# Performance work log

Measured on AMD Instinct MI355X. Metric: run time of the kernel, lower is better.

## Reference

```python
import jax, jax.numpy as jnp
import numpy as np

N = 50000        # nodes
E = 640000       # edges
D = 128          # emb_dim
L = 3            # num_layer
EDGE_DIM = 8
BN_EPS = 1e-5


def setup_inputs() -> dict:
    key = jax.random.key(0)
    ks = jax.random.split(key, 6)
    return dict(
        x=jax.random.normal(ks[0], (N, D), jnp.float32),
        edge_index=jax.random.randint(ks[1], (2, E), 0, N),
        edge_attr=jax.random.normal(ks[2], (E, EDGE_DIM), jnp.float32),
        eps=jnp.zeros((L,), jnp.float32),
        We=jax.random.normal(ks[3], (L, EDGE_DIM, D), jnp.float32) * 0.1,
        be=jnp.zeros((L, D), jnp.float32),
        W1=jax.random.normal(ks[4], (L, D, 2 * D), jnp.float32) * (1.0 / np.sqrt(D)),
        b1=jnp.zeros((L, 2 * D), jnp.float32),
        g1=jnp.ones((L, 2 * D), jnp.float32),
        bt1=jnp.zeros((L, 2 * D), jnp.float32),
        W2=jax.random.normal(ks[5], (L, 2 * D, D), jnp.float32) * (1.0 / np.sqrt(2 * D)),
        b2=jnp.zeros((L, D), jnp.float32),
        gbn=jnp.ones((L, D), jnp.float32),
        bbn=jnp.zeros((L, D), jnp.float32),
    )


def _bn(h, g, b):
    # BatchNorm1d, training-mode statistics over the node/batch axis
    mu = h.mean(axis=0)
    var = h.var(axis=0)
    return (h - mu) * jax.lax.rsqrt(var + BN_EPS) * g + b


def reference(x, edge_index, edge_attr, eps, We, be, W1, b1, g1, bt1, W2, b2, gbn, bbn):
    src, dst = edge_index[0], edge_index[1]
    h = x
    for l in range(L):
        # GINConv: edge-encoded messages, relu, scatter-add aggregation
        ee = edge_attr @ We[l] + be[l]                      # [E, D]
        msg = jax.nn.relu(h[src] + ee)                      # [E, D]
        agg = jax.ops.segment_sum(msg, dst, num_segments=N)  # [N, D]
        z = (1.0 + eps[l]) * h + agg
        # GIN MLP: Linear -> BN -> ReLU -> Linear
        z = jax.nn.relu(_bn(z @ W1[l] + b1[l], g1[l], bt1[l]))
        z = z @ W2[l] + b2[l]
        # outer per-layer BatchNorm; ReLU on all but the last layer (dropout = eval identity)
        z = _bn(z, gbn[l], bbn[l])
        if l < L - 1:
            z = jax.nn.relu(z)
        h = z  # residual=False, so no skip add
    return h  # JK == 'last'
```

## Files before the change

### kernel.cpp

```cpp
#include <hip/hip_runtime.h>

#define N_NODES 50000
#define N_EDGES 640000
#define D 128
#define D2 256
#define BN_EPS 1e-5f

typedef unsigned short ushort_t;
typedef unsigned int uint_t;

using bf16x8 = __attribute__((ext_vector_type(8))) short;
using f32x4  = __attribute__((ext_vector_type(4))) float;

__device__ inline ushort_t f2bf(float f) {
    uint_t u = __builtin_bit_cast(uint_t, f);
    u = (u + 0x7fffu + ((u >> 16) & 1u)) >> 16;
    return (ushort_t)u;
}
__device__ inline float bf2f(uint_t bits_lo16) {
    return __builtin_bit_cast(float, bits_lo16 << 16);
}

__global__ __launch_bounds__(256) void hist_kernel(
    const int* __restrict__ dst, int* __restrict__ hist)
{
    const int e = blockIdx.x * 256 + threadIdx.x;
    if (e < N_EDGES) atomicAdd(&hist[dst[e]], 1);
}

__global__ __launch_bounds__(256) void scan1_kernel(
    const int* __restrict__ hist, int* __restrict__ scanA,
    int* __restrict__ bsum)
{
    __shared__ int sm[256];
    const int t = threadIdx.x;
    const int idx = blockIdx.x * 256 + t;
    int val = (idx < N_NODES) ? hist[idx] : 0;
    sm[t] = val;
    __syncthreads();
#pragma unroll
    for (int off = 1; off < 256; off <<= 1) {
        const int add = (t >= off) ? sm[t - off] : 0;
        __syncthreads();
        val += add;
        sm[t] = val;
        __syncthreads();
    }
    scanA[idx] = val;
    if (t == 255) bsum[blockIdx.x] = val;
}

__global__ __launch_bounds__(256) void scan2_kernel(
    const int* __restrict__ bsum, int* __restrict__ bscan, int nb)
{
    __shared__ int sm[256];
    const int t = threadIdx.x;
    int val = (t < nb) ? bsum[t] : 0;
    sm[t] = val;
    __syncthreads();
#pragma unroll
    for (int off = 1; off < 256; off <<= 1) {
        const int add = (t >= off) ? sm[t - off] : 0;
        __syncthreads();
        val += add;
        sm[t] = val;
        __syncthreads();
    }
    bscan[t] = val;
}

__global__ __launch_bounds__(256) void scan3_kernel(
    const int* __restrict__ hist, const int* __restrict__ scanA,
    const int* __restrict__ bscan, int* __restrict__ excl)
{
    const int idx = blockIdx.x * 256 + threadIdx.x;
    if (idx < N_NODES) {
        const int carry = blockIdx.x ? bscan[blockIdx.x - 1] : 0;
        const int incl = scanA[idx] + carry;
        excl[idx] = incl - hist[idx];
        if (idx == N_NODES - 1) excl[N_NODES] = incl;
    }
}

__global__ __launch_bounds__(256) void scatter_kernel(
    const int* __restrict__ src, const int* __restrict__ dst,
    int* __restrict__ cursor, int* __restrict__ srcp_s,
    int* __restrict__ eperm)
{
    const int e = blockIdx.x * 256 + threadIdx.x;
    if (e < N_EDGES) {
        const int t = dst[e];
        const int p = atomicAdd(&cursor[t], 1);
        srcp_s[p] = src[e];
        eperm[p] = e;
    }
}

__global__ __launch_bounds__(256) void wtrans_kernel(
    const float* __restrict__ in, ushort_t* __restrict__ out, int K, int Nt)
{
    __shared__ float tile[32][33];
    const int l = blockIdx.z;
    in  += (size_t)l * K * Nt;
    out += (size_t)l * K * Nt;
    const int n0 = blockIdx.x * 32, k0 = blockIdx.y * 32;
    const int tx = threadIdx.x & 31, ty = threadIdx.x >> 5;
#pragma unroll
    for (int i = 0; i < 32; i += 8)
        tile[ty + i][tx] = in[(size_t)(k0 + ty + i) * Nt + n0 + tx];
    __syncthreads();
#pragma unroll
    for (int i = 0; i < 32; i += 8)
        out[(size_t)(n0 + ty + i) * K + k0 + tx] = f2bf(tile[tx][ty + i]);
}

__global__ __launch_bounds__(256) void agg_z_kernel(
    const float* __restrict__ h, const int* __restrict__ excl,
    const int* __restrict__ srcp_s, const int* __restrict__ eperm,
    const float* __restrict__ ea, const float* __restrict__ We_l,
    const float* __restrict__ be_l, const float* __restrict__ eps_l,
    ushort_t* __restrict__ z)
{
    const int lane = threadIdx.x & 63;
    const int wave = threadIdx.x >> 6;
    const int node = blockIdx.x * 4 + wave;
    const int grp  = lane >> 4;
    const int gl   = lane & 15;
    const int d0   = gl * 8;

    float wv[8][8];
#pragma unroll
    for (int k = 0; k < 8; ++k) {
        *(float4*)&wv[k][0] = *(const float4*)&We_l[k * D + d0];
        *(float4*)&wv[k][4] = *(const float4*)&We_l[k * D + d0 + 4];
    }
    float bev[8];
    *(float4*)&bev[0] = *(const float4*)&be_l[d0];
    *(float4*)&bev[4] = *(const float4*)&be_l[d0 + 4];

    const int p0 = excl[node];
    const int p1 = excl[node + 1];
    float acc[8] = {0.f, 0.f, 0.f, 0.f, 0.f, 0.f, 0.f, 0.f};

    for (int p = p0 + grp; p < p1; p += 4) {
        const int e = eperm[p];
        const int s = srcp_s[p];
        float eav[8];
        *(float4*)&eav[0] = *(const float4*)&ea[(size_t)e * 8];
        *(float4*)&eav[4] = *(const float4*)&ea[(size_t)e * 8 + 4];
        float hv[8];
        *(float4*)&hv[0] = *(const float4*)&h[(size_t)s * D + d0];
        *(float4*)&hv[4] = *(const float4*)&h[(size_t)s * D + d0 + 4];
        float m[8];
#pragma unroll
        for (int j = 0; j < 8; ++j) m[j] = bev[j];
#pragma unroll
        for (int k = 0; k < 8; ++k)
#pragma unroll
            for (int j = 0; j < 8; ++j)
                m[j] = fmaf(eav[k], wv[k][j], m[j]);
#pragma unroll
        for (int j = 0; j < 8; ++j)
            acc[j] += fmaxf(hv[j] + m[j], 0.f);
    }

#pragma unroll
    for (int j = 0; j < 8; ++j) {
        acc[j] += __shfl_xor(acc[j], 16);
        acc[j] += __shfl_xor(acc[j], 32);
    }

    if (grp == 0) {
        const float epsv = 1.0f + eps_l[0];
        float hn[8];
        *(float4*)&hn[0] = *(const float4*)&h[(size_t)node * D + d0];
        *(float4*)&hn[4] = *(const float4*)&h[(size_t)node * D + d0 + 4];
        uint4 o;
        uint_t w0 = (uint_t)f2bf(fmaf(epsv, hn[0], acc[0]));
        uint_t w1 = (uint_t)f2bf(fmaf(epsv, hn[1], acc[1]));
        uint_t w2 = (uint_t)f2bf(fmaf(epsv, hn[2], acc[2]));
        uint_t w3 = (uint_t)f2bf(fmaf(epsv, hn[3], acc[3]));
        uint_t w4 = (uint_t)f2bf(fmaf(epsv, hn[4], acc[4]));
        uint_t w5 = (uint_t)f2bf(fmaf(epsv, hn[5], acc[5]));
        uint_t w6 = (uint_t)f2bf(fmaf(epsv, hn[6], acc[6]));
        uint_t w7 = (uint_t)f2bf(fmaf(epsv, hn[7], acc[7]));
        o.x = w0 | (w1 << 16);
        o.y = w2 | (w3 << 16);
        o.z = w4 | (w5 << 16);
        o.w = w6 | (w7 << 16);
        *(uint4*)&z[(size_t)node * D + d0] = o;
    }
}

template<int KTILES>
__global__ __launch_bounds__(256) void gemm_bf16_kernel(
    const ushort_t* __restrict__ A, const ushort_t* __restrict__ Bt,
    const float* __restrict__ bias, ushort_t* __restrict__ out,
    float* __restrict__ gsum, float* __restrict__ gsq)
{
    __shared__ ushort_t As[128][136];
    __shared__ ushort_t Bs[128][136];
    __shared__ float ls_sum[128], ls_sq[128];
    const int tid = threadIdx.x;
    const int M0 = blockIdx.x * 128;
    const int N0 = blockIdx.y * 128;
    const int Ntot = gridDim.y * 128;
    const int K = KTILES * 128;
    if (tid < 128) { ls_sum[tid] = 0.f; ls_sq[tid] = 0.f; }
    const int lane = tid & 63, w = tid >> 6;
    const int wm = w >> 1, wn = w & 1;
    const int lr = lane & 15;
    const int lk = (lane >> 4) * 8;
    f32x4 acc[4][4] = {};

    for (int kt = 0; kt < KTILES; ++kt) {
        if (kt) __syncthreads();
#pragma unroll
        for (int p = 0; p < 8; ++p) {
            const int idx = p * 256 + tid;
            const int row = idx >> 4, ch = (idx & 15) * 8;
            uint4 v = make_uint4(0, 0, 0, 0);
            const int gr = M0 + row;
            if (gr < N_NODES)
                v = *(const uint4*)&A[(size_t)gr * K + kt * 128 + ch];
            *(uint4*)&As[row][ch] = v;
        }
#pragma unroll
        for (int p = 0; p < 8; ++p) {
            const int idx = p * 256 + tid;
            const int row = idx >> 4, ch = (idx & 15) * 8;
            *(uint4*)&Bs[row][ch] =
                *(const uint4*)&Bt[(size_t)(N0 + row) * K + kt * 128 + ch];
        }
        __syncthreads();
#pragma unroll
        for (int ks = 0; ks < 4; ++ks) {
            const int kof = ks * 32 + lk;
            bf16x8 af[4], bfr[4];
#pragma unroll
            for (int mi = 0; mi < 4; ++mi)
                af[mi] = *(const bf16x8*)&As[wm * 64 + mi * 16 + lr][kof];
#pragma unroll
            for (int ni = 0; ni < 4; ++ni)
                bfr[ni] = *(const bf16x8*)&Bs[wn * 64 + ni * 16 + lr][kof];
#pragma unroll
            for (int mi = 0; mi < 4; ++mi)
#pragma unroll
                for (int ni = 0; ni < 4; ++ni)
                    acc[mi][ni] = __builtin_amdgcn_mfma_f32_16x16x32_bf16(
                        af[mi], bfr[ni], acc[mi][ni], 0, 0, 0);
        }
    }
    __syncthreads();

#pragma unroll
    for (int ni = 0; ni < 4; ++ni) {
        const int cl = wn * 64 + ni * 16 + lr;
        const float bv = bias[N0 + cl];
        float ps = 0.f, pq = 0.f;
#pragma unroll
        for (int mi = 0; mi < 4; ++mi) {
            const int rbase = M0 + wm * 64 + mi * 16 + (lane >> 4) * 4;
#pragma unroll
            for (int r = 0; r < 4; ++r) {
                const int row = rbase + r;
                if (row < N_NODES) {
                    const float v = acc[mi][ni][r] + bv;
                    out[(size_t)row * Ntot + N0 + cl] = f2bf(v);
                    ps += v;
                    pq += v * v;
                }
            }
        }
        atomicAdd(&ls_sum[cl], ps);
        atomicAdd(&ls_sq[cl], pq);
    }
    __syncthreads();
    if (tid < 128) {
        unsafeAtomicAdd(&gsum[N0 + tid], ls_sum[tid]);
        unsafeAtomicAdd(&gsq[N0 + tid], ls_sq[tid]);
    }
}

__global__ void bnparam_kernel(const float* __restrict__ gsum,
                               const float* __restrict__ gsq,
                               const float* __restrict__ g,
                               const float* __restrict__ bt,
                               float* __restrict__ scale,
                               float* __restrict__ shift, int C)
{
    const int c = threadIdx.x;
    if (c < C) {
        const float inv_n = 1.0f / (float)N_NODES;
        const float mu = gsum[c] * inv_n;
        const float var = gsq[c] * inv_n - mu * mu;
        const float s = g[c] * rsqrtf(var + BN_EPS);
        scale[c] = s;
        shift[c] = bt[c] - mu * s;
    }
}

__global__ __launch_bounds__(256) void bnapply1_kernel(
    const ushort_t* __restrict__ t, const float* __restrict__ sc,
    const float* __restrict__ sh, ushort_t* __restrict__ u)
{
    const size_t idx = (size_t)blockIdx.x * 256 + threadIdx.x;
    const int c = (int)(idx & 31) * 8;
    const uint4 v = ((const uint4*)t)[idx];
    const float4 s0 = *(const float4*)&sc[c];
    const float4 s1 = *(const float4*)&sc[c + 4];
    const float4 h0 = *(const float4*)&sh[c];
    const float4 h1 = *(const float4*)&sh[c + 4];
    float f[8];
    f[0] = bf2f(v.x & 0xffffu); f[1] = bf2f(v.x >> 16);
    f[2] = bf2f(v.y & 0xffffu); f[3] = bf2f(v.y >> 16);
    f[4] = bf2f(v.z & 0xffffu); f[5] = bf2f(v.z >> 16);
    f[6] = bf2f(v.w & 0xffffu); f[7] = bf2f(v.w >> 16);
    f[0] = fmaxf(fmaf(f[0], s0.x, h0.x), 0.f);
    f[1] = fmaxf(fmaf(f[1], s0.y, h0.y), 0.f);
    f[2] = fmaxf(fmaf(f[2], s0.z, h0.z), 0.f);
    f[3] = fmaxf(fmaf(f[3], s0.w, h0.w), 0.f);
    f[4] = fmaxf(fmaf(f[4], s1.x, h1.x), 0.f);
    f[5] = fmaxf(fmaf(f[5], s1.y, h1.y), 0.f);
    f[6] = fmaxf(fmaf(f[6], s1.z, h1.z), 0.f);
    f[7] = fmaxf(fmaf(f[7], s1.w, h1.w), 0.f);
    uint4 o;
    o.x = (uint_t)f2bf(f[0]) | ((uint_t)f2bf(f[1]) << 16);
    o.y = (uint_t)f2bf(f[2]) | ((uint_t)f2bf(f[3]) << 16);
    o.z = (uint_t)f2bf(f[4]) | ((uint_t)f2bf(f[5]) << 16);
    o.w = (uint_t)f2bf(f[6]) | ((uint_t)f2bf(f[7]) << 16);
    ((uint4*)u)[idx] = o;
}

__global__ __launch_bounds__(256) void bnapply2_kernel(
    const ushort_t* __restrict__ t, const float* __restrict__ sc,
    const float* __restrict__ sh, float* __restrict__ outp, const int relu)
{
    const size_t idx = (size_t)blockIdx.x * 256 + threadIdx.x;
    const int c = (int)(idx & 15) * 8;
    const uint4 v = ((const uint4*)t)[idx];
    const float4 s0 = *(const float4*)&sc[c];
    const float4 s1 = *(const float4*)&sc[c + 4];
    const float4 h0 = *(const float4*)&sh[c];
    const float4 h1 = *(const float4*)&sh[c + 4];
    float4 r0, r1;
    r0.x = fmaf(bf2f(v.x & 0xffffu), s0.x, h0.x);
    r0.y = fmaf(bf2f(v.x >> 16),     s0.y, h0.y);
    r0.z = fmaf(bf2f(v.y & 0xffffu), s0.z, h0.z);
    r0.w = fmaf(bf2f(v.y >> 16),     s0.w, h0.w);
    r1.x = fmaf(bf2f(v.z & 0xffffu), s1.x, h1.x);
    r1.y = fmaf(bf2f(v.z >> 16),     s1.y, h1.y);
    r1.z = fmaf(bf2f(v.w & 0xffffu), s1.z, h1.z);
    r1.w = fmaf(bf2f(v.w >> 16),     s1.w, h1.w);
    if (relu) {
        r0.x = fmaxf(r0.x, 0.f); r0.y = fmaxf(r0.y, 0.f);
        r0.z = fmaxf(r0.z, 0.f); r0.w = fmaxf(r0.w, 0.f);
        r1.x = fmaxf(r1.x, 0.f); r1.y = fmaxf(r1.y, 0.f);
        r1.z = fmaxf(r1.z, 0.f); r1.w = fmaxf(r1.w, 0.f);
    }
    *(float4*)&outp[idx * 8]     = r0;
    *(float4*)&outp[idx * 8 + 4] = r1;
}

extern "C" void kernel_launch(void* const* d_in, const int* in_sizes, int n_in,
                              void* d_out, int out_size, void* d_ws, size_t ws_size,
                              hipStream_t stream)
{
    const float* x         = (const float*)d_in[0];
    const int*   edge_index= (const int*)d_in[1];
    const float* edge_attr = (const float*)d_in[2];
    const float* eps       = (const float*)d_in[3];
    const float* We        = (const float*)d_in[4];
    const float* be        = (const float*)d_in[5];
    const float* W1        = (const float*)d_in[6];
    const float* b1        = (const float*)d_in[7];
    const float* g1        = (const float*)d_in[8];
    const float* bt1       = (const float*)d_in[9];
    const float* W2        = (const float*)d_in[10];
    const float* b2        = (const float*)d_in[11];
    const float* gbn       = (const float*)d_in[12];
    const float* bbn       = (const float*)d_in[13];
    float* out = (float*)d_out;

    float* ws = (float*)d_ws;
    const size_t ND = (size_t)N_NODES * D;
    float* P1   = ws;
    float* P2   = P1 + ND;
    float* ZT2  = P2 + ND;
    float* T1   = ZT2 + ND;
    float* STATS = T1 + (size_t)N_NODES * D2;
    float* gsum1 = STATS;
    float* gsq1  = gsum1 + 3 * 256;
    float* gsum2 = gsq1 + 3 * 256;
    float* gsq2  = gsum2 + 3 * 128;
    float* scale1 = gsq2 + 3 * 128;
    float* shift1 = scale1 + 256;
    float* scale2 = shift1 + 256;
    float* shift2 = scale2 + 128;

    ushort_t* zbuf  = (ushort_t*)ZT2;
    ushort_t* t2buf = zbuf + ND;
    ushort_t* t1buf = (ushort_t*)T1;
    ushort_t* ubuf  = t1buf + (size_t)N_NODES * D2;

    int* hist   = (int*)T1;
    int* scanA  = hist + N_NODES;
    int* bsum   = scanA + 50176;
    int* bscan  = bsum + 256;
    int* cursor = bscan + 256;

    int* srcp_s = (int*)d_out;
    int* eperm  = srcp_s + N_EDGES;
    int* excl   = eperm + N_EDGES;
    ushort_t* W1t = (ushort_t*)((int*)d_out + 1330004);
    ushort_t* W2t = W1t + 3 * D2 * D;

    const int* srcp = edge_index;
    const int* dstp = edge_index + N_EDGES;

    hipMemsetAsync(STATS, 0, 2304 * sizeof(float), stream);
    hipMemsetAsync(hist, 0, N_NODES * sizeof(int), stream);

    const int EB = (N_EDGES + 255) / 256;
    const int NB = (N_NODES + 255) / 256;
    hist_kernel<<<EB, 256, 0, stream>>>(dstp, hist);
    scan1_kernel<<<NB, 256, 0, stream>>>(hist, scanA, bsum);
    scan2_kernel<<<1, 256, 0, stream>>>(bsum, bscan, NB);
    scan3_kernel<<<NB, 256, 0, stream>>>(hist, scanA, bscan, excl);
    hipMemcpyAsync(cursor, excl, N_NODES * sizeof(int),
                   hipMemcpyDeviceToDevice, stream);
    scatter_kernel<<<EB, 256, 0, stream>>>(srcp, dstp, cursor, srcp_s, eperm);

    wtrans_kernel<<<dim3(8, 4, 3), 256, 0, stream>>>(W1, W1t, D, D2);
    wtrans_kernel<<<dim3(4, 8, 3), 256, 0, stream>>>(W2, W2t, D2, D);

    const float* h_cur = x;
    float* houtbuf[3] = {P1, P2, out};

    for (int l = 0; l < 3; ++l) {
        agg_z_kernel<<<N_NODES / 4, 256, 0, stream>>>(
            h_cur, excl, srcp_s, eperm, edge_attr,
            We + (size_t)l * 8 * D, be + (size_t)l * D, eps + l, zbuf);

        dim3 grid1((N_NODES + 127) / 128, 2);
        gemm_bf16_kernel<1><<<grid1, 256, 0, stream>>>(
            zbuf, W1t + (size_t)l * D2 * D, b1 + (size_t)l * D2,
            t1buf, gsum1 + l * 256, gsq1 + l * 256);

        bnparam_kernel<<<1, 256, 0, stream>>>(
            gsum1 + l * 256, gsq1 + l * 256,
            g1 + (size_t)l * D2, bt1 + (size_t)l * D2, scale1, shift1, D2);

        bnapply1_kernel<<<(N_NODES * D2 / 8) / 256, 256, 0, stream>>>(
            t1buf, scale1, shift1, ubuf);

        dim3 grid2((N_NODES + 127) / 128, 1);
        gemm_bf16_kernel<2><<<grid2, 256, 0, stream>>>(
            ubuf, W2t + (size_t)l * D * D2, b2 + (size_t)l * D,
            t2buf, gsum2 + l * 128, gsq2 + l * 128);

        bnparam_kernel<<<1, 256, 0, stream>>>(
            gsum2 + l * 128, gsq2 + l * 128,
            gbn + (size_t)l * D, bbn + (size_t)l * D, scale2, shift2, D);

        bnapply2_kernel<<<(N_NODES * D / 8) / 256, 256, 0, stream>>>(
            t2buf, scale2, shift2, houtbuf[l], l < 2 ? 1 : 0);

        h_cur = houtbuf[l];
    }
}
```

Baseline: 711.2 us.

## Fuse BN apply into GEMM2 and aggregation, pre-permute edge attributes

Removes the separate BN1-apply and per-layer BN2-apply passes. BN1+ReLU is now applied while GEMM2 loads its A tile, and BN2+ReLU is applied on the fly to bf16 t2 rows gathered in the next layer's aggregation. Only one final bnapply2 runs, writing the fp32 output. Edge attributes are permuted into destination-sorted order during the scatter, so the aggregation reads them contiguously instead of through eperm. The aggregation loop is also unrolled by two edges. The cost is that gathered neighbor features are now read in bf16 precision, and every gathered row repeats the BN math.

```diff
diff --git a/kernel.cpp b/kernel.cpp
--- a/kernel.cpp
+++ b/kernel.cpp
@@ -84,15 +84,16 @@
 
 __global__ __launch_bounds__(256) void scatter_kernel(
     const int* __restrict__ src, const int* __restrict__ dst,
-    int* __restrict__ cursor, int* __restrict__ srcp_s,
-    int* __restrict__ eperm)
+    const float* __restrict__ ea, int* __restrict__ cursor,
+    int* __restrict__ srcp_s, float* __restrict__ ea_s)
 {
     const int e = blockIdx.x * 256 + threadIdx.x;
     if (e < N_EDGES) {
         const int t = dst[e];
         const int p = atomicAdd(&cursor[t], 1);
         srcp_s[p] = src[e];
-        eperm[p] = e;
+        *(float4*)&ea_s[(size_t)p * 8]     = *(const float4*)&ea[(size_t)e * 8];
+        *(float4*)&ea_s[(size_t)p * 8 + 4] = *(const float4*)&ea[(size_t)e * 8 + 4];
     }
 }
 
@@ -114,12 +115,59 @@
         out[(size_t)(n0 + ty + i) * K + k0 + tx] = f2bf(tile[tx][ty + i]);
 }
 
-__global__ __launch_bounds__(256) void agg_z_kernel(
+__device__ __forceinline__ void msg_accum(
+    const float* __restrict__ hv, const float* __restrict__ eav,
+    const float (&wv)[8][8], const float* __restrict__ bev,
+    float* __restrict__ acc)
+{
+    float m[8];
+#pragma unroll
+    for (int j = 0; j < 8; ++j) m[j] = bev[j];
+#pragma unroll
+    for (int k = 0; k < 8; ++k)
+#pragma unroll
+        for (int j = 0; j < 8; ++j)
+            m[j] = fmaf(eav[k], wv[k][j], m[j]);
+#pragma unroll
+    for (int j = 0; j < 8; ++j)
+        acc[j] += fmaxf(hv[j] + m[j], 0.f);
+}
+
+__device__ __forceinline__ void unpack_bn_relu(
+    const uint4 v, const float* __restrict__ scv,
+    const float* __restrict__ shv, float* __restrict__ hv)
+{
+    float f[8];
+    f[0] = bf2f(v.x & 0xffffu); f[1] = bf2f(v.x >> 16);
+    f[2] = bf2f(v.y & 0xffffu); f[3] = bf2f(v.y >> 16);
+    f[4] = bf2f(v.z & 0xffffu); f[5] = bf2f(v.z >> 16);
+    f[6] = bf2f(v.w & 0xffffu); f[7] = bf2f(v.w >> 16);
+#pragma unroll
+    for (int j = 0; j < 8; ++j)
+        hv[j] = fmaxf(fmaf(f[j], scv[j], shv[j]), 0.f);
+}
+
+__device__ __forceinline__ void store_z(
+    ushort_t* __restrict__ z, int node, int d0, float epsv,
+    const float* __restrict__ hn, const float* __restrict__ acc)
+{
+    uint_t w[8];
+#pragma unroll
+    for (int j = 0; j < 8; ++j)
+        w[j] = (uint_t)f2bf(fmaf(epsv, hn[j], acc[j]));
+    uint4 o;
+    o.x = w[0] | (w[1] << 16);
+    o.y = w[2] | (w[3] << 16);
+    o.z = w[4] | (w[5] << 16);
+    o.w = w[6] | (w[7] << 16);
+    *(uint4*)&z[(size_t)node * D + d0] = o;
+}
+
+__global__ __launch_bounds__(256) void agg_z_f32_kernel(
     const float* __restrict__ h, const int* __restrict__ excl,
-    const int* __restrict__ srcp_s, const int* __restrict__ eperm,
-    const float* __restrict__ ea, const float* __restrict__ We_l,
-    const float* __restrict__ be_l, const float* __restrict__ eps_l,
-    ushort_t* __restrict__ z)
+    const int* __restrict__ srcp_s, const float* __restrict__ ea_s,
+    const float* __restrict__ We_l, const float* __restrict__ be_l,
+    const float* __restrict__ eps_l, ushort_t* __restrict__ z)
 {
     const int lane = threadIdx.x & 63;
     const int wave = threadIdx.x >> 6;
@@ -142,26 +190,30 @@
     const int p1 = excl[node + 1];
     float acc[8] = {0.f, 0.f, 0.f, 0.f, 0.f, 0.f, 0.f, 0.f};
 
-    for (int p = p0 + grp; p < p1; p += 4) {
-        const int e = eperm[p];
-        const int s = srcp_s[p];
-        float eav[8];
-        *(float4*)&eav[0] = *(const float4*)&ea[(size_t)e * 8];
-        *(float4*)&eav[4] = *(const float4*)&ea[(size_t)e * 8 + 4];
-        float hv[8];
-        *(float4*)&hv[0] = *(const float4*)&h[(size_t)s * D + d0];
-        *(float4*)&hv[4] = *(const float4*)&h[(size_t)s * D + d0 + 4];
-        float m[8];
-#pragma unroll
-        for (int j = 0; j < 8; ++j) m[j] = bev[j];
-#pragma unroll
-        for (int k = 0; k < 8; ++k)
-#pragma unroll
-            for (int j = 0; j < 8; ++j)
-                m[j] = fmaf(eav[k], wv[k][j], m[j]);
-#pragma unroll
-        for (int j = 0; j < 8; ++j)
-            acc[j] += fmaxf(hv[j] + m[j], 0.f);
+    int p = p0 + grp;
+    for (; p + 4 < p1; p += 8) {
+        const int sA = srcp_s[p];
+        const int sB = srcp_s[p + 4];
+        float eA[8], eB[8], hA[8], hB[8];
+        *(float4*)&eA[0] = *(const float4*)&ea_s[(size_t)p * 8];
+        *(float4*)&eA[4] = *(const float4*)&ea_s[(size_t)p * 8 + 4];
+        *(float4*)&eB[0] = *(const float4*)&ea_s[(size_t)(p + 4) * 8];
+        *(float4*)&eB[4] = *(const float4*)&ea_s[(size_t)(p + 4) * 8 + 4];
+        *(float4*)&hA[0] = *(const float4*)&h[(size_t)sA * D + d0];
+        *(float4*)&hA[4] = *(const float4*)&h[(size_t)sA * D + d0 + 4];
+        *(float4*)&hB[0] = *(const float4*)&h[(size_t)sB * D + d0];
+        *(float4*)&hB[4] = *(const float4*)&h[(size_t)sB * D + d0 + 4];
+        msg_accum(hA, eA, wv, bev, acc);
+        msg_accum(hB, eB, wv, bev, acc);
+    }
+    if (p < p1) {
+        const int sA = srcp_s[p];
+        float eA[8], hA[8];
+        *(float4*)&eA[0] = *(const float4*)&ea_s[(size_t)p * 8];
+        *(float4*)&eA[4] = *(const float4*)&ea_s[(size_t)p * 8 + 4];
+        *(float4*)&hA[0] = *(const float4*)&h[(size_t)sA * D + d0];
+        *(float4*)&hA[4] = *(const float4*)&h[(size_t)sA * D + d0 + 4];
+        msg_accum(hA, eA, wv, bev, acc);
     }
 
 #pragma unroll
@@ -171,24 +223,83 @@
     }
 
     if (grp == 0) {
-        const float epsv = 1.0f + eps_l[0];
         float hn[8];
         *(float4*)&hn[0] = *(const float4*)&h[(size_t)node * D + d0];
         *(float4*)&hn[4] = *(const float4*)&h[(size_t)node * D + d0 + 4];
-        uint4 o;
-        uint_t w0 = (uint_t)f2bf(fmaf(epsv, hn[0], acc[0]));
-        uint_t w1 = (uint_t)f2bf(fmaf(epsv, hn[1], acc[1]));
-        uint_t w2 = (uint_t)f2bf(fmaf(epsv, hn[2], acc[2]));
-        uint_t w3 = (uint_t)f2bf(fmaf(epsv, hn[3], acc[3]));
-        uint_t w4 = (uint_t)f2bf(fmaf(epsv, hn[4], acc[4]));
-        uint_t w5 = (uint_t)f2bf(fmaf(epsv, hn[5], acc[5]));
-        uint_t w6 = (uint_t)f2bf(fmaf(epsv, hn[6], acc[6]));
-        uint_t w7 = (uint_t)f2bf(fmaf(epsv, hn[7], acc[7]));
-        o.x = w0 | (w1 << 16);
-        o.y = w2 | (w3 << 16);
-        o.z = w4 | (w5 << 16);
-        o.w = w6 | (w7 << 16);
-        *(uint4*)&z[(size_t)node * D + d0] = o;
+        store_z(z, node, d0, 1.0f + eps_l[0], hn, acc);
+    }
+}
+
+__global__ __launch_bounds__(256) void agg_z_bf16_kernel(
+    const ushort_t* __restrict__ t2, const float* __restrict__ sc2,
+    const float* __restrict__ sh2, const int* __restrict__ excl,
+    const int* __restrict__ srcp_s, const float* __restrict__ ea_s,
+    const float* __restrict__ We_l, const float* __restrict__ be_l,
+    const float* __restrict__ eps_l, ushort_t* __restrict__ z)
+{
+    const int lane = threadIdx.x & 63;
+    const int wave = threadIdx.x >> 6;
+    const int node = blockIdx.x * 4 + wave;
+    const int grp  = lane >> 4;
+    const int gl   = lane & 15;
+    const int d0   = gl * 8;
+
+    float wv[8][8];
+#pragma unroll
+    for (int k = 0; k < 8; ++k) {
+        *(float4*)&wv[k][0] = *(const float4*)&We_l[k * D + d0];
+        *(float4*)&wv[k][4] = *(const float4*)&We_l[k * D + d0 + 4];
+    }
+    float bev[8], scv[8], shv[8];
+    *(float4*)&bev[0] = *(const float4*)&be_l[d0];
+    *(float4*)&bev[4] = *(const float4*)&be_l[d0 + 4];
+    *(float4*)&scv[0] = *(const float4*)&sc2[d0];
+    *(float4*)&scv[4] = *(const float4*)&sc2[d0 + 4];
+    *(float4*)&shv[0] = *(const float4*)&sh2[d0];
+    *(float4*)&shv[4] = *(const float4*)&sh2[d0 + 4];
+
+    const int p0 = excl[node];
+    const int p1 = excl[node + 1];
+    float acc[8] = {0.f, 0.f, 0.f, 0.f, 0.f, 0.f, 0.f, 0.f};
+
+    int p = p0 + grp;
+    for (; p + 4 < p1; p += 8) {
+        const int sA = srcp_s[p];
+        const int sB = srcp_s[p + 4];
+        float eA[8], eB[8];
+        *(float4*)&eA[0] = *(const float4*)&ea_s[(size_t)p * 8];
+        *(float4*)&eA[4] = *(const float4*)&ea_s[(size_t)p * 8 + 4];
+        *(float4*)&eB[0] = *(const float4*)&ea_s[(size_t)(p + 4) * 8];
+        *(float4*)&eB[4] = *(const float4*)&ea_s[(size_t)(p + 4) * 8 + 4];
+        const uint4 vA = *(const uint4*)&t2[(size_t)sA * D + d0];
+        const uint4 vB = *(const uint4*)&t2[(size_t)sB * D + d0];
+        float hA[8], hB[8];
+        unpack_bn_relu(vA, scv, shv, hA);
+        msg_accum(hA, eA, wv, bev, acc);
+        unpack_bn_relu(vB, scv, shv, hB);
+        msg_accum(hB, eB, wv, bev, acc);
+    }
+    if (p < p1) {
+        const int sA = srcp_s[p];
+        float eA[8], hA[8];
+        *(float4*)&eA[0] = *(const float4*)&ea_s[(size_t)p * 8];
+        *(float4*)&eA[4] = *(const float4*)&ea_s[(size_t)p * 8 + 4];
+        const uint4 vA = *(const uint4*)&t2[(size_t)sA * D + d0];
+        unpack_bn_relu(vA, scv, shv, hA);
+        msg_accum(hA, eA, wv, bev, acc);
+    }
+
+#pragma unroll
+    for (int j = 0; j < 8; ++j) {
+        acc[j] += __shfl_xor(acc[j], 16);
+        acc[j] += __shfl_xor(acc[j], 32);
+    }
+
+    if (grp == 0) {
+        const uint4 vN = *(const uint4*)&t2[(size_t)node * D + d0];
+        float hn[8];
+        unpack_bn_relu(vN, scv, shv, hn);
+        store_z(z, node, d0, 1.0f + eps_l[0], hn, acc);
     }
 }
 
@@ -282,6 +393,117 @@
     }
 }
 
+__global__ __launch_bounds__(256) void gemm2_bn_kernel(
+    const ushort_t* __restrict__ A, const float* __restrict__ sc1,
+    const float* __restrict__ sh1, const ushort_t* __restrict__ Bt,
+    const float* __restrict__ bias, ushort_t* __restrict__ out,
+    float* __restrict__ gsum, float* __restrict__ gsq)
+{
+    __shared__ ushort_t As[128][136];
+    __shared__ ushort_t Bs[128][136];
+    __shared__ float ls_sum[128], ls_sq[128];
+    const int tid = threadIdx.x;
+    const int M0 = blockIdx.x * 128;
+    const int K = 256, Ntot = 128;
+    if (tid < 128) { ls_sum[tid] = 0.f; ls_sq[tid] = 0.f; }
+    const int lane = tid & 63, w = tid >> 6;
+    const int wm = w >> 1, wn = w & 1;
+    const int lr = lane & 15;
+    const int lk = (lane >> 4) * 8;
+    f32x4 acc[4][4] = {};
+
+    for (int kt = 0; kt < 2; ++kt) {
+        if (kt) __syncthreads();
+#pragma unroll
+        for (int p = 0; p < 8; ++p) {
+            const int idx = p * 256 + tid;
+            const int row = idx >> 4, ch = (idx & 15) * 8;
+            const int col = kt * 128 + ch;
+            uint4 v = make_uint4(0, 0, 0, 0);
+            const int gr = M0 + row;
+            if (gr < N_NODES) {
+                const uint4 t = *(const uint4*)&A[(size_t)gr * K + col];
+                float f[8];
+                f[0] = bf2f(t.x & 0xffffu); f[1] = bf2f(t.x >> 16);
+                f[2] = bf2f(t.y & 0xffffu); f[3] = bf2f(t.y >> 16);
+                f[4] = bf2f(t.z & 0xffffu); f[5] = bf2f(t.z >> 16);
+                f[6] = bf2f(t.w & 0xffffu); f[7] = bf2f(t.w >> 16);
+                const float4 s0 = *(const float4*)&sc1[col];
+                const float4 s1 = *(const float4*)&sc1[col + 4];
+                const float4 h0 = *(const float4*)&sh1[col];
+                const float4 h1 = *(const float4*)&sh1[col + 4];
+                f[0] = fmaxf(fmaf(f[0], s0.x, h0.x), 0.f);
+                f[1] = fmaxf(fmaf(f[1], s0.y, h0.y), 0.f);
+                f[2] = fmaxf(fmaf(f[2], s0.z, h0.z), 0.f);
+                f[3] = fmaxf(fmaf(f[3], s0.w, h0.w), 0.f);
+                f[4] = fmaxf(fmaf(f[4], s1.x, h1.x), 0.f);
+                f[5] = fmaxf(fmaf(f[5], s1.y, h1.y), 0.f);
+                f[6] = fmaxf(fmaf(f[6], s1.z, h1.z), 0.f);
+                f[7] = fmaxf(fmaf(f[7], s1.w, h1.w), 0.f);
+                v.x = (uint_t)f2bf(f[0]) | ((uint_t)f2bf(f[1]) << 16);
+                v.y = (uint_t)f2bf(f[2]) | ((uint_t)f2bf(f[3]) << 16);
+                v.z = (uint_t)f2bf(f[4]) | ((uint_t)f2bf(f[5]) << 16);
+                v.w = (uint_t)f2bf(f[6]) | ((uint_t)f2bf(f[7]) << 16);
+            }
+            *(uint4*)&As[row][ch] = v;
+        }
+#pragma unroll
+        for (int p = 0; p < 8; ++p) {
+            const int idx = p * 256 + tid;
+            const int row = idx >> 4, ch = (idx & 15) * 8;
+            *(uint4*)&Bs[row][ch] =
+                *(const uint4*)&Bt[(size_t)row * K + kt * 128 + ch];
+        }
+        __syncthreads();
+#pragma unroll
+        for (int ks = 0; ks < 4; ++ks) {
+            const int kof = ks * 32 + lk;
+            bf16x8 af[4], bfr[4];
+#pragma unroll
+            for (int mi = 0; mi < 4; ++mi)
+                af[mi] = *(const bf16x8*)&As[wm * 64 + mi * 16 + lr][kof];
+#pragma unroll
+            for (int ni = 0; ni < 4; ++ni)
+                bfr[ni] = *(const bf16x8*)&Bs[wn * 64 + ni * 16 + lr][kof];
+#pragma unroll
+            for (int mi = 0; mi < 4; ++mi)
+#pragma unroll
+                for (int ni = 0; ni < 4; ++ni)
+                    acc[mi][ni] = __builtin_amdgcn_mfma_f32_16x16x32_bf16(
+                        af[mi], bfr[ni], acc[mi][ni], 0, 0, 0);
+        }
+    }
+    __syncthreads();
+
+#pragma unroll
+    for (int ni = 0; ni < 4; ++ni) {
+        const int cl = wn * 64 + ni * 16 + lr;
+        const float bv = bias[cl];
+        float ps = 0.f, pq = 0.f;
+#pragma unroll
+        for (int mi = 0; mi < 4; ++mi) {
+            const int rbase = M0 + wm * 64 + mi * 16 + (lane >> 4) * 4;
+#pragma unroll
+            for (int r = 0; r < 4; ++r) {
+                const int row = rbase + r;
+                if (row < N_NODES) {
+                    const float v = acc[mi][ni][r] + bv;
+                    out[(size_t)row * Ntot + cl] = f2bf(v);
+                    ps += v;
+                    pq += v * v;
+                }
+            }
+        }
+        atomicAdd(&ls_sum[cl], ps);
+        atomicAdd(&ls_sq[cl], pq);
+    }
+    __syncthreads();
+    if (tid < 128) {
+        unsafeAtomicAdd(&gsum[tid], ls_sum[tid]);
+        unsafeAtomicAdd(&gsq[tid], ls_sq[tid]);
+    }
+}
+
 __global__ void bnparam_kernel(const float* __restrict__ gsum,
                                const float* __restrict__ gsq,
                                const float* __restrict__ g,
@@ -300,41 +522,9 @@
     }
 }
 
-__global__ __launch_bounds__(256) void bnapply1_kernel(
-    const ushort_t* __restrict__ t, const float* __restrict__ sc,
-    const float* __restrict__ sh, ushort_t* __restrict__ u)
-{
-    const size_t idx = (size_t)blockIdx.x * 256 + threadIdx.x;
-    const int c = (int)(idx & 31) * 8;
-    const uint4 v = ((const uint4*)t)[idx];
-    const float4 s0 = *(const float4*)&sc[c];
-    const float4 s1 = *(const float4*)&sc[c + 4];
-    const float4 h0 = *(const float4*)&sh[c];
-    const float4 h1 = *(const float4*)&sh[c + 4];
-    float f[8];
-    f[0] = bf2f(v.x & 0xffffu); f[1] = bf2f(v.x >> 16);
-    f[2] = bf2f(v.y & 0xffffu); f[3] = bf2f(v.y >> 16);
-    f[4] = bf2f(v.z & 0xffffu); f[5] = bf2f(v.z >> 16);
-    f[6] = bf2f(v.w & 0xffffu); f[7] = bf2f(v.w >> 16);
-    f[0] = fmaxf(fmaf(f[0], s0.x, h0.x), 0.f);
-    f[1] = fmaxf(fmaf(f[1], s0.y, h0.y), 0.f);
-    f[2] = fmaxf(fmaf(f[2], s0.z, h0.z), 0.f);
-    f[3] = fmaxf(fmaf(f[3], s0.w, h0.w), 0.f);
-    f[4] = fmaxf(fmaf(f[4], s1.x, h1.x), 0.f);
-    f[5] = fmaxf(fmaf(f[5], s1.y, h1.y), 0.f);
-    f[6] = fmaxf(fmaf(f[6], s1.z, h1.z), 0.f);
-    f[7] = fmaxf(fmaf(f[7], s1.w, h1.w), 0.f);
-    uint4 o;
-    o.x = (uint_t)f2bf(f[0]) | ((uint_t)f2bf(f[1]) << 16);
-    o.y = (uint_t)f2bf(f[2]) | ((uint_t)f2bf(f[3]) << 16);
-    o.z = (uint_t)f2bf(f[4]) | ((uint_t)f2bf(f[5]) << 16);
-    o.w = (uint_t)f2bf(f[6]) | ((uint_t)f2bf(f[7]) << 16);
-    ((uint4*)u)[idx] = o;
-}
-
 __global__ __launch_bounds__(256) void bnapply2_kernel(
     const ushort_t* __restrict__ t, const float* __restrict__ sc,
-    const float* __restrict__ sh, float* __restrict__ outp, const int relu)
+    const float* __restrict__ sh, float* __restrict__ outp)
 {
     const size_t idx = (size_t)blockIdx.x * 256 + threadIdx.x;
     const int c = (int)(idx & 15) * 8;
@@ -352,12 +542,6 @@
     r1.y = fmaf(bf2f(v.z >> 16),     s1.y, h1.y);
     r1.z = fmaf(bf2f(v.w & 0xffffu), s1.z, h1.z);
     r1.w = fmaf(bf2f(v.w >> 16),     s1.w, h1.w);
-    if (relu) {
-        r0.x = fmaxf(r0.x, 0.f); r0.y = fmaxf(r0.y, 0.f);
-        r0.z = fmaxf(r0.z, 0.f); r0.w = fmaxf(r0.w, 0.f);
-        r1.x = fmaxf(r1.x, 0.f); r1.y = fmaxf(r1.y, 0.f);
-        r1.z = fmaxf(r1.z, 0.f); r1.w = fmaxf(r1.w, 0.f);
-    }
     *(float4*)&outp[idx * 8]     = r0;
     *(float4*)&outp[idx * 8 + 4] = r1;
 }
@@ -384,35 +568,33 @@
 
     float* ws = (float*)d_ws;
     const size_t ND = (size_t)N_NODES * D;
-    float* P1   = ws;
-    float* P2   = P1 + ND;
-    float* ZT2  = P2 + ND;
-    float* T1   = ZT2 + ND;
-    float* STATS = T1 + (size_t)N_NODES * D2;
+    float* EAS  = ws;
+    float* ZB   = EAS + (size_t)N_EDGES * 8;
+    float* T2B  = ZB + ND / 2;
+    float* T1B  = T2B + ND / 2;
+    float* STATS = T1B + ND;
     float* gsum1 = STATS;
     float* gsq1  = gsum1 + 3 * 256;
     float* gsum2 = gsq1 + 3 * 256;
     float* gsq2  = gsum2 + 3 * 128;
     float* scale1 = gsq2 + 3 * 128;
     float* shift1 = scale1 + 256;
-    float* scale2 = shift1 + 256;
-    float* shift2 = scale2 + 128;
-
-    ushort_t* zbuf  = (ushort_t*)ZT2;
-    ushort_t* t2buf = zbuf + ND;
-    ushort_t* t1buf = (ushort_t*)T1;
-    ushort_t* ubuf  = t1buf + (size_t)N_NODES * D2;
-
-    int* hist   = (int*)T1;
+    float* sc2buf = shift1 + 256;
+    float* sh2buf = sc2buf + 3 * 128;
+
+    ushort_t* zbuf  = (ushort_t*)ZB;
+    ushort_t* t2buf = (ushort_t*)T2B;
+    ushort_t* t1buf = (ushort_t*)T1B;
+
+    int* hist   = (int*)T1B;
     int* scanA  = hist + N_NODES;
     int* bsum   = scanA + 50176;
     int* bscan  = bsum + 256;
     int* cursor = bscan + 256;
 
     int* srcp_s = (int*)d_out;
-    int* eperm  = srcp_s + N_EDGES;
-    int* excl   = eperm + N_EDGES;
-    ushort_t* W1t = (ushort_t*)((int*)d_out + 1330004);
+    int* excl   = srcp_s + N_EDGES;
+    ushort_t* W1t = (ushort_t*)((int*)d_out + 690008);
     ushort_t* W2t = W1t + 3 * D2 * D;
 
     const int* srcp = edge_index;
@@ -429,18 +611,23 @@
     scan3_kernel<<<NB, 256, 0, stream>>>(hist, scanA, bscan, excl);
     hipMemcpyAsync(cursor, excl, N_NODES * sizeof(int),
                    hipMemcpyDeviceToDevice, stream);
-    scatter_kernel<<<EB, 256, 0, stream>>>(srcp, dstp, cursor, srcp_s, eperm);
+    scatter_kernel<<<EB, 256, 0, stream>>>(srcp, dstp, edge_attr,
+                                           cursor, srcp_s, EAS);
 
     wtrans_kernel<<<dim3(8, 4, 3), 256, 0, stream>>>(W1, W1t, D, D2);
     wtrans_kernel<<<dim3(4, 8, 3), 256, 0, stream>>>(W2, W2t, D2, D);
 
-    const float* h_cur = x;
-    float* houtbuf[3] = {P1, P2, out};
-
     for (int l = 0; l < 3; ++l) {
-        agg_z_kernel<<<N_NODES / 4, 256, 0, stream>>>(
-            h_cur, excl, srcp_s, eperm, edge_attr,
-            We + (size_t)l * 8 * D, be + (size_t)l * D, eps + l, zbuf);
+        if (l == 0) {
+            agg_z_f32_kernel<<<N_NODES / 4, 256, 0, stream>>>(
+                x, excl, srcp_s, EAS,
+                We + (size_t)l * 8 * D, be + (size_t)l * D, eps + l, zbuf);
+        } else {
+            agg_z_bf16_kernel<<<N_NODES / 4, 256, 0, stream>>>(
+                t2buf, sc2buf + (l - 1) * 128, sh2buf + (l - 1) * 128,
+                excl, srcp_s, EAS,
+                We + (size_t)l * 8 * D, be + (size_t)l * D, eps + l, zbuf);
+        }
 
         dim3 grid1((N_NODES + 127) / 128, 2);
         gemm_bf16_kernel<1><<<grid1, 256, 0, stream>>>(
@@ -451,21 +638,18 @@
             gsum1 + l * 256, gsq1 + l * 256,
             g1 + (size_t)l * D2, bt1 + (size_t)l * D2, scale1, shift1, D2);
 
-        bnapply1_kernel<<<(N_NODES * D2 / 8) / 256, 256, 0, stream>>>(
-            t1buf, scale1, shift1, ubuf);
-
         dim3 grid2((N_NODES + 127) / 128, 1);
-        gemm_bf16_kernel<2><<<grid2, 256, 0, stream>>>(
-            ubuf, W2t + (size_t)l * D * D2, b2 + (size_t)l * D,
-            t2buf, gsum2 + l * 128, gsq2 + l * 128);
+        gemm2_bn_kernel<<<grid2, 256, 0, stream>>>(
+            t1buf, scale1, shift1,
+            W2t + (size_t)l * D * D2, b2 + (size_t)l * D, t2buf,
+            gsum2 + l * 128, gsq2 + l * 128);
 
         bnparam_kernel<<<1, 256, 0, stream>>>(
             gsum2 + l * 128, gsq2 + l * 128,
-            gbn + (size_t)l * D, bbn + (size_t)l * D, scale2, shift2, D);
-
-        bnapply2_kernel<<<(N_NODES * D / 8) / 256, 256, 0, stream>>>(
-            t2buf, scale2, shift2, houtbuf[l], l < 2 ? 1 : 0);
-
-        h_cur = houtbuf[l];
-    }
-}
+            gbn + (size_t)l * D, bbn + (size_t)l * D,
+            sc2buf + l * 128, sh2buf + l * 128, D);
+    }
+
+    bnapply2_kernel<<<(N_NODES * D / 8) / 256, 256, 0, stream>>>(
+        t2buf, sc2buf + 2 * 128, sh2buf + 2 * 128, out);
+}
```

Result: faster. 675.7 us (-5.0%).
